# Optimization experiments

Measured on AMD Instinct MI355X. Metric: run time of the kernel, lower is better.

## Reference

```python
import jax, jax.numpy as jnp
import numpy as np

V, H, B, T = 100000, 512, 4096, 524288
EPS = 1e-5

def setup_inputs() -> dict:
    key = jax.random.key(0)
    ks = jax.random.split(key, 8)
    tokens = jax.random.randint(ks[0], (T,), 0, V, dtype=jnp.int32)
    seg_ids = jnp.sort(jax.random.randint(ks[1], (T,), 0, B, dtype=jnp.int32))
    t = jax.random.bernoulli(ks[2], 0.5, (B,)).astype(jnp.float32)
    emb = jax.random.normal(ks[3], (V, H), dtype=jnp.float32) * 0.1
    W1 = jax.random.normal(ks[4], (H, H), dtype=jnp.float32) * (1.0 / np.sqrt(H))
    b1 = jnp.zeros((H,), jnp.float32)
    gamma = jnp.ones((H,), jnp.float32)
    beta = jnp.zeros((H,), jnp.float32)
    w2 = jax.random.normal(ks[5], (H,), dtype=jnp.float32) * (1.0 / np.sqrt(H))
    b2 = jnp.zeros((), jnp.float32)
    return {"tokens": tokens, "seg_ids": seg_ids, "t": t, "emb": emb,
            "W1": W1, "b1": b1, "gamma": gamma, "beta": beta, "w2": w2, "b2": b2}

def reference(tokens, seg_ids, t, emb, W1, b1, gamma, beta, w2, b2):
    nb = t.shape[0]
    # fused gather + segment-mean (bag-of-words), replaces the per-sample loop
    gathered = emb[tokens]  # [T, H]
    sums = jax.ops.segment_sum(gathered, seg_ids, num_segments=nb)  # [B, H]
    counts = jax.ops.segment_sum(jnp.ones((tokens.shape[0],), jnp.float32), seg_ids, num_segments=nb)
    bow = sums / jnp.maximum(counts, 1.0)[:, None]  # [B, H]
    # Linear -> BatchNorm1d (training-mode batch stats, biased var) -> ReLU
    z = bow @ W1.T + b1  # [B, H]
    mu = jnp.mean(z, axis=0)
    var = jnp.mean((z - mu) ** 2, axis=0)
    zn = (z - mu) * jax.lax.rsqrt(var + EPS) * gamma + beta
    h = jax.nn.relu(zn)  # dropout treated as identity (eval mode) for determinism
    logits = h @ w2 + b2  # [B]
    # BCEWithLogitsLoss: mean(softplus(logit) - t*logit), numerically stable
    loss = jnp.mean(jnp.logaddexp(0.0, logits) - t * logits)
    return (loss, logits)
```

## Files before the change

### kernel.cpp

```cpp
#include <hip/hip_runtime.h>
#include <hip/hip_bf16.h>
#include <hip/hip_fp16.h>
#include <math.h>

constexpr int NTOK = 524288;
constexpr int NB   = 4096;
constexpr int H    = 512;
constexpr float EPS = 1e-5f;

typedef _Float16 half8 __attribute__((ext_vector_type(8)));
typedef float f32x4 __attribute__((ext_vector_type(4)));
struct h4 { __half2 a, b; };

__global__ __launch_bounds__(256) void k_convert(
    const float* __restrict__ src, h4* __restrict__ dst) {
  size_t i = (size_t)blockIdx.x * 256 + threadIdx.x;
  float4 v = ((const float4*)src)[i];
  h4 o;
  o.a = __floats2half2_rn(v.x, v.y);
  o.b = __floats2half2_rn(v.z, v.w);
  dst[i] = o;
}

__global__ __launch_bounds__(256) void k_gather_mean(
    const int* __restrict__ tokens, const int* __restrict__ seg,
    const half8* __restrict__ embh, half8* __restrict__ bow_h) {
  const int b = blockIdx.x;
  int lo = 0, hi = NTOK;
  while (lo < hi) { int mid = (lo + hi) >> 1; if (seg[mid] < b) lo = mid + 1; else hi = mid; }
  const int start = lo;
  hi = NTOK;
  while (lo < hi) { int mid = (lo + hi) >> 1; if (seg[mid] < b + 1) lo = mid + 1; else hi = mid; }
  const int end = lo;

  const int tid = threadIdx.x;
  const int lane = tid & 63;
  const int g = tid >> 6;

  float acc[8] = {};
  int i = start + g;
  for (; i + 12 < end; i += 16) {
    half8 v0 = embh[(size_t)tokens[i]      * 64 + lane];
    half8 v1 = embh[(size_t)tokens[i + 4]  * 64 + lane];
    half8 v2 = embh[(size_t)tokens[i + 8]  * 64 + lane];
    half8 v3 = embh[(size_t)tokens[i + 12] * 64 + lane];
#pragma unroll
    for (int j = 0; j < 8; ++j)
      acc[j] += (float)v0[j] + (float)v1[j] + (float)v2[j] + (float)v3[j];
  }
  for (; i < end; i += 4) {
    half8 v0 = embh[(size_t)tokens[i] * 64 + lane];
#pragma unroll
    for (int j = 0; j < 8; ++j) acc[j] += (float)v0[j];
  }

  __shared__ float part[3][64][9];
  if (g > 0) {
#pragma unroll
    for (int j = 0; j < 8; ++j) part[g - 1][lane][j] = acc[j];
  }
  __syncthreads();
  if (g == 0) {
    const int cnt = end - start;
    const float s = 1.0f / (float)(cnt > 0 ? cnt : 1);
    half8 o;
#pragma unroll
    for (int j = 0; j < 8; ++j) {
      float v = acc[j] + part[0][lane][j] + part[1][lane][j] + part[2][lane][j];
      o[j] = (_Float16)(v * s);
    }
    bow_h[(size_t)b * 64 + lane] = o;
  }
}

__global__ __launch_bounds__(256) void k_gemm_mfma(
    const _Float16* __restrict__ A,
    const _Float16* __restrict__ Bw,
    const float* __restrict__ b1, float* __restrict__ C) {
  const int tid = threadIdx.x;
  const int lane = tid & 63;
  const int gw = blockIdx.x * 4 + (tid >> 6);
  const int m0 = (gw >> 3) * 16;
  const int n0 = (gw & 7) * 64;
  const int l15 = lane & 15, quad = lane >> 4;

  f32x4 acc0 = {}, acc1 = {}, acc2 = {}, acc3 = {};
  const _Float16* ap = A + (size_t)(m0 + l15) * H + quad * 8;
  const _Float16* bp = Bw + (size_t)(n0 + l15) * H + quad * 8;

#pragma unroll
  for (int k = 0; k < H; k += 32) {
    half8 af  = *(const half8*)(ap + k);
    half8 bf0 = *(const half8*)(bp + k);
    half8 bf1 = *(const half8*)(bp + 16 * H + k);
    half8 bf2 = *(const half8*)(bp + 32 * H + k);
    half8 bf3 = *(const half8*)(bp + 48 * H + k);
    acc0 = __builtin_amdgcn_mfma_f32_16x16x32_f16(af, bf0, acc0, 0, 0, 0);
    acc1 = __builtin_amdgcn_mfma_f32_16x16x32_f16(af, bf1, acc1, 0, 0, 0);
    acc2 = __builtin_amdgcn_mfma_f32_16x16x32_f16(af, bf2, acc2, 0, 0, 0);
    acc3 = __builtin_amdgcn_mfma_f32_16x16x32_f16(af, bf3, acc3, 0, 0, 0);
  }

  const float bn0v = b1[n0 + l15];
  const float bn1v = b1[n0 + 16 + l15];
  const float bn2v = b1[n0 + 32 + l15];
  const float bn3v = b1[n0 + 48 + l15];
  float* crow = C + (size_t)(m0 + quad * 4) * H + n0 + l15;
#pragma unroll
  for (int r = 0; r < 4; ++r) {
    crow[(size_t)r * H]      = acc0[r] + bn0v;
    crow[(size_t)r * H + 16] = acc1[r] + bn1v;
    crow[(size_t)r * H + 32] = acc2[r] + bn2v;
    crow[(size_t)r * H + 48] = acc3[r] + bn3v;
  }
}

__global__ __launch_bounds__(256) void k_colstats(
    const float* __restrict__ z, float* __restrict__ ps, float* __restrict__ pss) {
  const int blk = blockIdx.x;
  const int c0 = threadIdx.x * 2;
  const int r0 = blk * 64;
  float s0 = 0, s1 = 0, q0 = 0, q1 = 0;
  for (int r = 0; r < 64; ++r) {
    float2 v = *(const float2*)&z[(size_t)(r0 + r) * H + c0];
    s0 += v.x; s1 += v.y;
    q0 += v.x * v.x; q1 += v.y * v.y;
  }
  ps[blk * H + c0] = s0; ps[blk * H + c0 + 1] = s1;
  pss[blk * H + c0] = q0; pss[blk * H + c0 + 1] = q1;
}

__global__ __launch_bounds__(128) void k_finalize(
    const float* __restrict__ ps, const float* __restrict__ pss,
    const float* __restrict__ gamma, const float* __restrict__ beta,
    float* __restrict__ scale, float* __restrict__ shift) {
  const int c = blockIdx.x * 128 + threadIdx.x;
  float s = 0, q = 0;
#pragma unroll 8
  for (int i = 0; i < 64; ++i) { s += ps[i * H + c]; q += pss[i * H + c]; }
  const float mu = s * (1.0f / NB);
  const float var = q * (1.0f / NB) - mu * mu;
  const float rstd = rsqrtf(var + EPS);
  const float sc = rstd * gamma[c];
  scale[c] = sc;
  shift[c] = beta[c] - mu * sc;
}

__global__ __launch_bounds__(256) void k_bn_dot(
    const float* __restrict__ z, const float* __restrict__ scale,
    const float* __restrict__ shift, const float* __restrict__ w2,
    const float* __restrict__ b2, float* __restrict__ out) {
  const int tid = threadIdx.x;
  const int wave = tid >> 6, lane = tid & 63;
  const int b = blockIdx.x * 4 + wave;
  const float4* __restrict__ z4 = (const float4*)(z + (size_t)b * H);
  const float4* __restrict__ sc4 = (const float4*)scale;
  const float4* __restrict__ sh4 = (const float4*)shift;
  const float4* __restrict__ w24 = (const float4*)w2;
  float acc = 0.f;
#pragma unroll
  for (int i = lane; i < 128; i += 64) {
    float4 zv = z4[i], sc = sc4[i], sh = sh4[i], w = w24[i];
    float h0 = fmaxf(zv.x * sc.x + sh.x, 0.f);
    float h1 = fmaxf(zv.y * sc.y + sh.y, 0.f);
    float h2 = fmaxf(zv.z * sc.z + sh.z, 0.f);
    float h3 = fmaxf(zv.w * sc.w + sh.w, 0.f);
    acc += h0 * w.x + h1 * w.y + h2 * w.z + h3 * w.w;
  }
#pragma unroll
  for (int off = 32; off > 0; off >>= 1) acc += __shfl_down(acc, off, 64);
  if (lane == 0) out[1 + b] = acc + b2[0];
}

__global__ __launch_bounds__(1024) void k_loss(
    const float* __restrict__ t, float* __restrict__ d_out) {
  const int tid = threadIdx.x;
  float s = 0.f;
#pragma unroll
  for (int b = tid; b < NB; b += 1024) {
    float x = d_out[1 + b];
    float sp = fmaxf(x, 0.f) + log1pf(expf(-fabsf(x)));
    s += sp - t[b] * x;
  }
  __shared__ float red[1024];
  red[tid] = s;
  __syncthreads();
  for (int off = 512; off > 0; off >>= 1) {
    if (tid < off) red[tid] += red[tid + off];
    __syncthreads();
  }
  if (tid == 0) d_out[0] = red[0] * (1.0f / NB);
}

extern "C" void kernel_launch(void* const* d_in, const int* in_sizes, int n_in,
                              void* d_out, int out_size, void* d_ws, size_t ws_size,
                              hipStream_t stream) {
  const int*   tokens = (const int*)d_in[0];
  const int*   seg    = (const int*)d_in[1];
  const float* t      = (const float*)d_in[2];
  const float* emb    = (const float*)d_in[3];
  const float* W1     = (const float*)d_in[4];
  const float* b1     = (const float*)d_in[5];
  const float* gamma  = (const float*)d_in[6];
  const float* beta   = (const float*)d_in[7];
  const float* w2     = (const float*)d_in[8];
  const float* b2     = (const float*)d_in[9];
  float* out = (float*)d_out;

  char* wsb = (char*)d_ws;
  half8*    embh  = (half8*)wsb;
  _Float16* W1h   = (_Float16*)(wsb + 102400000);
  half8*    bow_h = (half8*)(wsb + 102924288);
  float*    z     = (float*)(wsb + 107118592);
  float*    ps    = (float*)(wsb + 115507200);
  float*    pss   = ps + 64 * H;
  float*    scale = pss + 64 * H;
  float*    shift = scale + H;

  k_convert<<<50000, 256, 0, stream>>>(emb, (h4*)embh);
  k_convert<<<256, 256, 0, stream>>>(W1, (h4*)W1h);
  k_gather_mean<<<NB, 256, 0, stream>>>(tokens, seg, embh, bow_h);
  k_gemm_mfma<<<512, 256, 0, stream>>>((const _Float16*)bow_h, W1h, b1, z);
  k_colstats<<<64, 256, 0, stream>>>(z, ps, pss);
  k_finalize<<<4, 128, 0, stream>>>(ps, pss, gamma, beta, scale, shift);
  k_bn_dot<<<NB / 4, 256, 0, stream>>>(z, scale, shift, w2, b2, out);
  k_loss<<<1, 1024, 0, stream>>>(t, out);
}
```

Before: 420.1 us.

## Merge conversions, precompute segment bounds, widen colstats, fuse loss into bn_dot

Merges the two fp32-to-fp16 conversion launches into one and uses nontemporal loads for the embedding table. Replaces the per-block binary searches with a separate boundary-scan kernel. Splits the column statistics over 256 blocks instead of 64, and folds the BCE loss into the bn_dot kernel through atomicAdd, with finalize zeroing the output first. This removes launches and serial work, at the cost of nondeterministic float atomic summation and a larger finalize reduction.

```diff
diff --git a/kernel.cpp b/kernel.cpp
--- a/kernel.cpp
+++ b/kernel.cpp
@@ -10,28 +10,47 @@
 
 typedef _Float16 half8 __attribute__((ext_vector_type(8)));
 typedef float f32x4 __attribute__((ext_vector_type(4)));
+typedef float fvec4 __attribute__((ext_vector_type(4)));
 struct h4 { __half2 a, b; };
 
 __global__ __launch_bounds__(256) void k_convert(
-    const float* __restrict__ src, h4* __restrict__ dst) {
-  size_t i = (size_t)blockIdx.x * 256 + threadIdx.x;
-  float4 v = ((const float4*)src)[i];
-  h4 o;
-  o.a = __floats2half2_rn(v.x, v.y);
-  o.b = __floats2half2_rn(v.z, v.w);
-  dst[i] = o;
+    const float* __restrict__ emb, h4* __restrict__ embh,
+    const float* __restrict__ W1, h4* __restrict__ W1h) {
+  const size_t bid = blockIdx.x;
+  if (bid < 50000) {
+    size_t i = bid * 256 + threadIdx.x;
+    fvec4 v = __builtin_nontemporal_load((const fvec4*)emb + i);
+    h4 o;
+    o.a = __floats2half2_rn(v[0], v[1]);
+    o.b = __floats2half2_rn(v[2], v[3]);
+    embh[i] = o;
+  } else {
+    size_t i = (bid - 50000) * 256 + threadIdx.x;
+    fvec4 v = *((const fvec4*)W1 + i);
+    h4 o;
+    o.a = __floats2half2_rn(v[0], v[1]);
+    o.b = __floats2half2_rn(v[2], v[3]);
+    W1h[i] = o;
+  }
+}
+
+__global__ __launch_bounds__(256) void k_bounds(
+    const int* __restrict__ seg, int* __restrict__ starts) {
+  const int i = blockIdx.x * 256 + threadIdx.x;
+  const int cur = seg[i];
+  const int prev = (i == 0) ? -1 : seg[i - 1];
+  for (int b = prev + 1; b <= cur; ++b) starts[b] = i;
+  if (i == NTOK - 1) {
+    for (int b = cur + 1; b <= NB; ++b) starts[b] = NTOK;
+  }
 }
 
 __global__ __launch_bounds__(256) void k_gather_mean(
-    const int* __restrict__ tokens, const int* __restrict__ seg,
+    const int* __restrict__ tokens, const int* __restrict__ starts,
     const half8* __restrict__ embh, half8* __restrict__ bow_h) {
   const int b = blockIdx.x;
-  int lo = 0, hi = NTOK;
-  while (lo < hi) { int mid = (lo + hi) >> 1; if (seg[mid] < b) lo = mid + 1; else hi = mid; }
-  const int start = lo;
-  hi = NTOK;
-  while (lo < hi) { int mid = (lo + hi) >> 1; if (seg[mid] < b + 1) lo = mid + 1; else hi = mid; }
-  const int end = lo;
+  const int start = starts[b];
+  const int end = starts[b + 1];
 
   const int tid = threadIdx.x;
   const int lane = tid & 63;
@@ -119,9 +138,10 @@
     const float* __restrict__ z, float* __restrict__ ps, float* __restrict__ pss) {
   const int blk = blockIdx.x;
   const int c0 = threadIdx.x * 2;
-  const int r0 = blk * 64;
+  const int r0 = blk * 16;
   float s0 = 0, s1 = 0, q0 = 0, q1 = 0;
-  for (int r = 0; r < 64; ++r) {
+#pragma unroll
+  for (int r = 0; r < 16; ++r) {
     float2 v = *(const float2*)&z[(size_t)(r0 + r) * H + c0];
     s0 += v.x; s1 += v.y;
     q0 += v.x * v.x; q1 += v.y * v.y;
@@ -133,11 +153,13 @@
 __global__ __launch_bounds__(128) void k_finalize(
     const float* __restrict__ ps, const float* __restrict__ pss,
     const float* __restrict__ gamma, const float* __restrict__ beta,
-    float* __restrict__ scale, float* __restrict__ shift) {
+    float* __restrict__ scale, float* __restrict__ shift,
+    float* __restrict__ out) {
   const int c = blockIdx.x * 128 + threadIdx.x;
+  if (c == 0) out[0] = 0.f;
   float s = 0, q = 0;
 #pragma unroll 8
-  for (int i = 0; i < 64; ++i) { s += ps[i * H + c]; q += pss[i * H + c]; }
+  for (int i = 0; i < 256; ++i) { s += ps[i * H + c]; q += pss[i * H + c]; }
   const float mu = s * (1.0f / NB);
   const float var = q * (1.0f / NB) - mu * mu;
   const float rstd = rsqrtf(var + EPS);
@@ -149,7 +171,8 @@
 __global__ __launch_bounds__(256) void k_bn_dot(
     const float* __restrict__ z, const float* __restrict__ scale,
     const float* __restrict__ shift, const float* __restrict__ w2,
-    const float* __restrict__ b2, float* __restrict__ out) {
+    const float* __restrict__ b2, const float* __restrict__ t,
+    float* __restrict__ out) {
   const int tid = threadIdx.x;
   const int wave = tid >> 6, lane = tid & 63;
   const int b = blockIdx.x * 4 + wave;
@@ -169,27 +192,16 @@
   }
 #pragma unroll
   for (int off = 32; off > 0; off >>= 1) acc += __shfl_down(acc, off, 64);
-  if (lane == 0) out[1 + b] = acc + b2[0];
-}
-
-__global__ __launch_bounds__(1024) void k_loss(
-    const float* __restrict__ t, float* __restrict__ d_out) {
-  const int tid = threadIdx.x;
-  float s = 0.f;
-#pragma unroll
-  for (int b = tid; b < NB; b += 1024) {
-    float x = d_out[1 + b];
-    float sp = fmaxf(x, 0.f) + log1pf(expf(-fabsf(x)));
-    s += sp - t[b] * x;
-  }
-  __shared__ float red[1024];
-  red[tid] = s;
+
+  __shared__ float ls[4];
+  if (lane == 0) {
+    const float logit = acc + b2[0];
+    out[1 + b] = logit;
+    const float sp = fmaxf(logit, 0.f) + log1pf(expf(-fabsf(logit)));
+    ls[wave] = (sp - t[b] * logit) * (1.0f / NB);
+  }
   __syncthreads();
-  for (int off = 512; off > 0; off >>= 1) {
-    if (tid < off) red[tid] += red[tid + off];
-    __syncthreads();
-  }
-  if (tid == 0) d_out[0] = red[0] * (1.0f / NB);
+  if (tid == 0) atomicAdd(out, ls[0] + ls[1] + ls[2] + ls[3]);
 }
 
 extern "C" void kernel_launch(void* const* d_in, const int* in_sizes, int n_in,
@@ -213,16 +225,16 @@
   half8*    bow_h = (half8*)(wsb + 102924288);
   float*    z     = (float*)(wsb + 107118592);
   float*    ps    = (float*)(wsb + 115507200);
-  float*    pss   = ps + 64 * H;
-  float*    scale = pss + 64 * H;
+  float*    pss   = ps + 256 * H;
+  float*    scale = pss + 256 * H;
   float*    shift = scale + H;
-
-  k_convert<<<50000, 256, 0, stream>>>(emb, (h4*)embh);
-  k_convert<<<256, 256, 0, stream>>>(W1, (h4*)W1h);
-  k_gather_mean<<<NB, 256, 0, stream>>>(tokens, seg, embh, bow_h);
+  int*      starts = (int*)(wsb + 116559872);
+
+  k_convert<<<50256, 256, 0, stream>>>(emb, (h4*)embh, W1, (h4*)W1h);
+  k_bounds<<<NTOK / 256, 256, 0, stream>>>(seg, starts);
+  k_gather_mean<<<NB, 256, 0, stream>>>(tokens, starts, embh, bow_h);
   k_gemm_mfma<<<512, 256, 0, stream>>>((const _Float16*)bow_h, W1h, b1, z);
-  k_colstats<<<64, 256, 0, stream>>>(z, ps, pss);
-  k_finalize<<<4, 128, 0, stream>>>(ps, pss, gamma, beta, scale, shift);
-  k_bn_dot<<<NB / 4, 256, 0, stream>>>(z, scale, shift, w2, b2, out);
-  k_loss<<<1, 1024, 0, stream>>>(t, out);
-}
+  k_colstats<<<256, 256, 0, stream>>>(z, ps, pss);
+  k_finalize<<<4, 128, 0, stream>>>(ps, pss, gamma, beta, scale, shift, out);
+  k_bn_dot<<<NB / 4, 256, 0, stream>>>(z, scale, shift, w2, b2, t, out);
+}
```

New measurement: 428.3 us. About the same (+2.0%).
